# Kernel tuning notes

Hardware: AMD Instinct MI355X
Metric: run time of the kernel (lower is better)

Reference implementation:

```python
import jax, jax.numpy as jnp
import numpy as np

N = 50000   # n_nodes
E = 800000  # n_edges (directed)
D = 64      # feature dim (in = hidden = out = 64 per source)


def setup_inputs() -> dict:
    key = jax.random.key(0)
    ks = jax.random.split(key, 16)
    s = 0.1  # init scale
    inp = {
        "x": jax.random.normal(ks[0], (N, D), jnp.float32),
        "edge_index": jax.random.randint(ks[1], (2, E), 0, N),
        # GCNConv 1
        "W1": jax.random.normal(ks[2], (D, 64), jnp.float32) * s,
        "b1": jnp.zeros((64,), jnp.float32),
        # TransformerConv (heads=1): query/key/value + root (skip) linear
        "Wq": jax.random.normal(ks[3], (64, 64), jnp.float32) * s,
        "bq": jnp.zeros((64,), jnp.float32),
        "Wk": jax.random.normal(ks[4], (64, 64), jnp.float32) * s,
        "bk": jnp.zeros((64,), jnp.float32),
        "Wv": jax.random.normal(ks[5], (64, 64), jnp.float32) * s,
        "bv": jnp.zeros((64,), jnp.float32),
        "Ws": jax.random.normal(ks[6], (64, 64), jnp.float32) * s,
        "bs": jnp.zeros((64,), jnp.float32),
        # GCNConv 2
        "W2": jax.random.normal(ks[7], (64, D), jnp.float32) * s,
        "b2": jnp.zeros((D,), jnp.float32),
    }
    return inp


def gcn_conv(x, W, b, src, dst, n):
    """PyG GCNConv: symmetric normalization with self-loops, then scatter-add."""
    xw = x @ W  # [N, F]
    loop = jnp.arange(n)
    src2 = jnp.concatenate([src, loop])
    dst2 = jnp.concatenate([dst, loop])
    deg = jax.ops.segment_sum(jnp.ones(src2.shape[0], xw.dtype), dst2, num_segments=n)
    dinv = jnp.where(deg > 0, jax.lax.rsqrt(deg), 0.0)
    norm = dinv[src2] * dinv[dst2]  # [E+N]
    out = jax.ops.segment_sum(xw[src2] * norm[:, None], dst2, num_segments=n)
    return out + b


def segment_softmax(logits, seg, n):
    m = jax.ops.segment_max(logits, seg, num_segments=n)
    e = jnp.exp(logits - m[seg])
    z = jax.ops.segment_sum(e, seg, num_segments=n)
    return e / z[seg]


def transformer_conv(x, Wq, bq, Wk, bk, Wv, bv, Ws, bs, src, dst, n):
    """PyG TransformerConv (heads=1, concat=True, root_weight=True)."""
    q = x @ Wq + bq  # [N, 64]
    k = x @ Wk + bk
    v = x @ Wv + bv
    scale = jax.lax.rsqrt(jnp.asarray(q.shape[-1], q.dtype))
    logits = jnp.sum(q[dst] * k[src], axis=-1) * scale  # [E]
    alpha = segment_softmax(logits, dst, n)
    aggr = jax.ops.segment_sum(v[src] * alpha[:, None], dst, num_segments=n)
    return aggr + x @ Ws + bs  # root/skip connection


def reference(x, edge_index, W1, b1, Wq, bq, Wk, bk, Wv, bv, Ws, bs, W2, b2):
    src, dst = edge_index[0], edge_index[1]
    n = x.shape[0]
    x1 = jax.nn.relu(gcn_conv(x, W1, b1, src, dst, n))
    x2 = transformer_conv(x1, Wq, bq, Wk, bk, Wv, bv, Ws, bs, src, dst, n)
    x3 = gcn_conv(x2, W2, b2, src, dst, n)
    return x3
```

## Files before the change

### kernel.cpp

```cpp
#include <hip/hip_runtime.h>
#include <math.h>


#define D 64
#define BKT_SHIFT 9
#define CAP 12288
#define CHUNK 4096

__device__ __forceinline__ unsigned short f2bf(float f) {
    unsigned int u = __float_as_uint(f);
    u += 0x7FFFu + ((u >> 16) & 1u);
    return (unsigned short)(u >> 16);
}
#define BF_LO(u) __uint_as_float((u) << 16)
#define BF_HI(u) __uint_as_float((u) & 0xFFFF0000u)


__global__ void init_gcursor(int* __restrict__ gcursor) {
    if (threadIdx.x < 128) gcursor[threadIdx.x] = 0;
}

__global__ __launch_bounds__(256) void binA_kernel(const int* __restrict__ src,
                                                   const int* __restrict__ dst,
                                                   int* __restrict__ gcursor,
                                                   unsigned int* __restrict__ staging,
                                                   int e, int nbkt) {
    __shared__ int cntB[128];
    __shared__ int offB[128];
    __shared__ int curB[128];
    __shared__ int gbase[128];
    __shared__ unsigned int pairs[CHUNK];
    __shared__ unsigned char bkt[CHUNK];

    int t = threadIdx.x;
    int e0 = blockIdx.x * CHUNK;
    int ecnt = min(CHUNK, e - e0);

    if (t < 128) cntB[t] = 0;
    __syncthreads();

    int myS[CHUNK / 256], myD[CHUNK / 256];
    #pragma unroll
    for (int i = 0; i < CHUNK / 256; ++i) {
        int idx = t + 256 * i;
        if (idx < ecnt) {
            myS[i] = src[e0 + idx];
            myD[i] = dst[e0 + idx];
            atomicAdd(&cntB[myD[i] >> BKT_SHIFT], 1);
        }
    }
    __syncthreads();
    if (t < 128) offB[t] = cntB[t];
    __syncthreads();
    for (int off = 1; off < 128; off <<= 1) {
        int add = (t < 128 && t >= off) ? offB[t - off] : 0;
        __syncthreads();
        if (t < 128) offB[t] += add;
        __syncthreads();
    }
    if (t < 128) {
        int excl = offB[t] - cntB[t];
        offB[t] = excl;
        curB[t] = excl;
        if (t < nbkt && cntB[t] > 0) gbase[t] = atomicAdd(&gcursor[t], cntB[t]);
    }
    __syncthreads();
    #pragma unroll
    for (int i = 0; i < CHUNK / 256; ++i) {
        int idx = t + 256 * i;
        if (idx < ecnt) {
            int b = myD[i] >> BKT_SHIFT;
            int p = atomicAdd(&curB[b], 1);
            pairs[p] = ((unsigned int)myD[i] << 16) | (unsigned int)myS[i];
            bkt[p] = (unsigned char)b;
        }
    }
    __syncthreads();
    for (int p = t; p < ecnt; p += 256) {
        int b = bkt[p];
        staging[(size_t)b * CAP + gbase[b] + (p - offB[b])] = pairs[p];
    }
}

__global__ __launch_bounds__(256) void binB_kernel(const int* __restrict__ gcursor,
                                                   const unsigned int* __restrict__ staging,
                                                   unsigned short* __restrict__ esrc,
                                                   int* __restrict__ cnt,
                                                   int* __restrict__ rowptr,
                                                   float* __restrict__ dinv,
                                                   int n, int nbkt) {
    __shared__ int bpre[128];
    __shared__ int c512[512];
    __shared__ int o512[512];
    int t = threadIdx.x;
    int b = blockIdx.x;

    if (t < 128) bpre[t] = (t < nbkt) ? gcursor[t] : 0;
    __syncthreads();
    for (int off = 1; off < 128; off <<= 1) {
        int add = (t < 128 && t >= off) ? bpre[t - off] : 0;
        __syncthreads();
        if (t < 128) bpre[t] += add;
        __syncthreads();
    }
    int base_b = (b == 0) ? 0 : bpre[b - 1];
    int cnt_b = gcursor[b];
    int lo = b << BKT_SHIFT;

    c512[t] = 0; c512[t + 256] = 0;
    __syncthreads();
    const unsigned int* st = staging + (size_t)b * CAP;
    for (int i = t; i < cnt_b; i += 256)
        atomicAdd(&c512[(int)(st[i] >> 16) - lo], 1);
    __syncthreads();
    o512[t] = c512[t]; o512[t + 256] = c512[t + 256];
    __syncthreads();
    for (int off = 1; off < 512; off <<= 1) {
        int a1 = (t >= off) ? o512[t - off] : 0;
        int a2 = o512[t + 256 - off];
        __syncthreads();
        o512[t] += a1; o512[t + 256] += a2;
        __syncthreads();
    }
    int e1 = o512[t] - c512[t];
    int e2 = o512[t + 256] - c512[t + 256];
    __syncthreads();
    o512[t] = e1; o512[t + 256] = e2;
    __syncthreads();
    for (int i = t; i < 512; i += 256) {
        int g = lo + i;
        if (g < n) {
            int c = c512[i];
            cnt[g] = c;
            rowptr[g] = base_b + o512[i];
            dinv[g] = rsqrtf((float)c + 1.0f);
        }
    }
    __syncthreads();
    for (int i = t; i < cnt_b; i += 256) {
        unsigned int pk = st[i];
        int local = (int)(pk >> 16) - lo;
        int p = atomicAdd(&o512[local], 1);
        esrc[base_b + p] = (unsigned short)(pk & 0xFFFFu);
    }
}

__global__ __launch_bounds__(256) void gemm64_bf16s(const float* __restrict__ X,
                                                    const float* __restrict__ W,
                                                    const float* __restrict__ dinv,
                                                    unsigned short* __restrict__ xs, int n) {
    __shared__ float sX[64][68];
    __shared__ float sW[64 * 64];
    int t = threadIdx.x;
    int base = blockIdx.x * 64;
    #pragma unroll
    for (int i = 0; i < 4; ++i) {
        int f = t * 4 + i * 1024;
        *(float4*)&sW[f] = *(const float4*)&W[f];
        int r = f >> 6, c = f & 63;
        int row = base + r;
        float4 xv = (row < n) ? *(const float4*)&X[(size_t)row * D + c]
                              : make_float4(0.f, 0.f, 0.f, 0.f);
        *(float4*)&sX[r][c] = xv;
    }
    __syncthreads();

    int cg = t & 15, rg = t >> 4;
    int j0 = cg * 4, r0 = rg * 4;
    float acc[4][4];
    #pragma unroll
    for (int a = 0; a < 4; ++a)
        #pragma unroll
        for (int c = 0; c < 4; ++c) acc[a][c] = 0.0f;

    #pragma unroll 4
    for (int kk = 0; kk < 64; kk += 4) {
        float4 w0 = *(const float4*)&sW[(kk + 0) * 64 + j0];
        float4 w1 = *(const float4*)&sW[(kk + 1) * 64 + j0];
        float4 w2 = *(const float4*)&sW[(kk + 2) * 64 + j0];
        float4 w3 = *(const float4*)&sW[(kk + 3) * 64 + j0];
        #pragma unroll
        for (int a = 0; a < 4; ++a) {
            float4 xv = *(const float4*)&sX[r0 + a][kk];
            acc[a][0] = fmaf(xv.x, w0.x, acc[a][0]); acc[a][1] = fmaf(xv.x, w0.y, acc[a][1]);
            acc[a][2] = fmaf(xv.x, w0.z, acc[a][2]); acc[a][3] = fmaf(xv.x, w0.w, acc[a][3]);
            acc[a][0] = fmaf(xv.y, w1.x, acc[a][0]); acc[a][1] = fmaf(xv.y, w1.y, acc[a][1]);
            acc[a][2] = fmaf(xv.y, w1.z, acc[a][2]); acc[a][3] = fmaf(xv.y, w1.w, acc[a][3]);
            acc[a][0] = fmaf(xv.z, w2.x, acc[a][0]); acc[a][1] = fmaf(xv.z, w2.y, acc[a][1]);
            acc[a][2] = fmaf(xv.z, w2.z, acc[a][2]); acc[a][3] = fmaf(xv.z, w2.w, acc[a][3]);
            acc[a][0] = fmaf(xv.w, w3.x, acc[a][0]); acc[a][1] = fmaf(xv.w, w3.y, acc[a][1]);
            acc[a][2] = fmaf(xv.w, w3.z, acc[a][2]); acc[a][3] = fmaf(xv.w, w3.w, acc[a][3]);
        }
    }

    #pragma unroll
    for (int a = 0; a < 4; ++a) {
        int row = base + r0 + a;
        if (row < n) {
            float dv = dinv[row];
            ushort4 h;
            h.x = f2bf(acc[a][0] * dv);
            h.y = f2bf(acc[a][1] * dv);
            h.z = f2bf(acc[a][2] * dv);
            h.w = f2bf(acc[a][3] * dv);
            *(ushort4*)&xs[(size_t)row * D + j0] = h;
        }
    }
}

__global__ __launch_bounds__(256) void fusedA_kernel(const unsigned short* __restrict__ xs,
                                                     const float* __restrict__ dinv,
                                                     const int* __restrict__ rowptr,
                                                     const int* __restrict__ cnt,
                                                     const unsigned short* __restrict__ esrc,
                                                     const float* __restrict__ b1,
                                                     const float* __restrict__ Wq,
                                                     const float* __restrict__ bq,
                                                     const float* __restrict__ Wk,
                                                     const float* __restrict__ bk,
                                                     const float* __restrict__ Wv,
                                                     const float* __restrict__ bv,
                                                     const float* __restrict__ Ws,
                                                     const float* __restrict__ bs,
                                                     float* __restrict__ Yq,
                                                     unsigned short* __restrict__ kv,
                                                     float* __restrict__ Ysk, int n) {
    __shared__ float sX[64][68];
    __shared__ float sW[64 * 64];
    int t = threadIdx.x;
    int base = blockIdx.x * 64;
    int wid = t >> 6, lane = t & 63;
    int grp = lane >> 3, sub = lane & 7;
    int j0 = sub * 8;

    float4 bb0 = *(const float4*)&b1[j0];
    float4 bb1 = *(const float4*)&b1[j0 + 4];

    #pragma unroll
    for (int slot = 0; slot < 2; ++slot) {
        int local = wid * 16 + slot * 8 + grp;
        int node = base + local;
        float a[8] = {0.f, 0.f, 0.f, 0.f, 0.f, 0.f, 0.f, 0.f};
        float4 o0 = make_float4(0.f, 0.f, 0.f, 0.f);
        float4 o1 = make_float4(0.f, 0.f, 0.f, 0.f);
        if (node < n) {
            float dd = dinv[node];
            int start = rowptr[node], deg = cnt[node];
            uint4 sr = *(const uint4*)&xs[(size_t)node * D + j0];
            a[0] += BF_LO(sr.x); a[1] += BF_HI(sr.x);
            a[2] += BF_LO(sr.y); a[3] += BF_HI(sr.y);
            a[4] += BF_LO(sr.z); a[5] += BF_HI(sr.z);
            a[6] += BF_LO(sr.w); a[7] += BF_HI(sr.w);
            int sNext = (deg > 0) ? esrc[start] : 0;
            for (int i = 0; i < deg; ++i) {
                int s = sNext;
                if (i + 1 < deg) sNext = esrc[start + i + 1];
                uint4 r = *(const uint4*)&xs[(size_t)s * D + j0];
                a[0] += BF_LO(r.x); a[1] += BF_HI(r.x);
                a[2] += BF_LO(r.y); a[3] += BF_HI(r.y);
                a[4] += BF_LO(r.z); a[5] += BF_HI(r.z);
                a[6] += BF_LO(r.w); a[7] += BF_HI(r.w);
            }
            o0.x = fmaxf(fmaf(dd, a[0], bb0.x), 0.f);
            o0.y = fmaxf(fmaf(dd, a[1], bb0.y), 0.f);
            o0.z = fmaxf(fmaf(dd, a[2], bb0.z), 0.f);
            o0.w = fmaxf(fmaf(dd, a[3], bb0.w), 0.f);
            o1.x = fmaxf(fmaf(dd, a[4], bb1.x), 0.f);
            o1.y = fmaxf(fmaf(dd, a[5], bb1.y), 0.f);
            o1.z = fmaxf(fmaf(dd, a[6], bb1.z), 0.f);
            o1.w = fmaxf(fmaf(dd, a[7], bb1.w), 0.f);
        }
        *(float4*)&sX[local][j0] = o0;
        *(float4*)&sX[local][j0 + 4] = o1;
    }

    int cg = t & 15, rg = t >> 4;
    int gj0 = cg * 4, r0 = rg * 4;

    #pragma unroll 1
    for (int w4 = 0; w4 < 4; ++w4) {
        const float* W = (w4 == 0) ? Wq : (w4 == 1) ? Wk : (w4 == 2) ? Wv : Ws;
        const float* B = (w4 == 0) ? bq : (w4 == 1) ? bk : (w4 == 2) ? bv : bs;
        __syncthreads();
        #pragma unroll
        for (int i = 0; i < 4; ++i) {
            int f = t * 4 + i * 1024;
            *(float4*)&sW[f] = *(const float4*)&W[f];
        }
        __syncthreads();

        float acc[4][4];
        #pragma unroll
        for (int a = 0; a < 4; ++a)
            #pragma unroll
            for (int c = 0; c < 4; ++c) acc[a][c] = 0.0f;

        #pragma unroll 4
        for (int kk = 0; kk < 64; kk += 4) {
            float4 w0 = *(const float4*)&sW[(kk + 0) * 64 + gj0];
            float4 w1 = *(const float4*)&sW[(kk + 1) * 64 + gj0];
            float4 w2 = *(const float4*)&sW[(kk + 2) * 64 + gj0];
            float4 w3 = *(const float4*)&sW[(kk + 3) * 64 + gj0];
            #pragma unroll
            for (int a = 0; a < 4; ++a) {
                float4 xv = *(const float4*)&sX[r0 + a][kk];
                acc[a][0] = fmaf(xv.x, w0.x, acc[a][0]); acc[a][1] = fmaf(xv.x, w0.y, acc[a][1]);
                acc[a][2] = fmaf(xv.x, w0.z, acc[a][2]); acc[a][3] = fmaf(xv.x, w0.w, acc[a][3]);
                acc[a][0] = fmaf(xv.y, w1.x, acc[a][0]); acc[a][1] = fmaf(xv.y, w1.y, acc[a][1]);
                acc[a][2] = fmaf(xv.y, w1.z, acc[a][2]); acc[a][3] = fmaf(xv.y, w1.w, acc[a][3]);
                acc[a][0] = fmaf(xv.z, w2.x, acc[a][0]); acc[a][1] = fmaf(xv.z, w2.y, acc[a][1]);
                acc[a][2] = fmaf(xv.z, w2.z, acc[a][2]); acc[a][3] = fmaf(xv.z, w2.w, acc[a][3]);
                acc[a][0] = fmaf(xv.w, w3.x, acc[a][0]); acc[a][1] = fmaf(xv.w, w3.y, acc[a][1]);
                acc[a][2] = fmaf(xv.w, w3.z, acc[a][2]); acc[a][3] = fmaf(xv.w, w3.w, acc[a][3]);
            }
        }

        float4 bb = *(const float4*)&B[gj0];
        if (w4 == 0) {
            #pragma unroll
            for (int a = 0; a < 4; ++a) {
                int row = base + r0 + a;
                if (row < n) {
                    float4 o = make_float4((acc[a][0] + bb.x) * 0.125f,
                                           (acc[a][1] + bb.y) * 0.125f,
                                           (acc[a][2] + bb.z) * 0.125f,
                                           (acc[a][3] + bb.w) * 0.125f);
                    *(float4*)&Yq[(size_t)row * D + gj0] = o;
                }
            }
        } else if (w4 == 3) {
            #pragma unroll
            for (int a = 0; a < 4; ++a) {
                int row = base + r0 + a;
                if (row < n) {
                    float4 o = make_float4(acc[a][0] + bb.x, acc[a][1] + bb.y,
                                           acc[a][2] + bb.z, acc[a][3] + bb.w);
                    *(float4*)&Ysk[(size_t)row * D + gj0] = o;
                }
            }
        } else {
            int off = (w4 == 1) ? 0 : 64;
            #pragma unroll
            for (int a = 0; a < 4; ++a) {
                int row = base + r0 + a;
                if (row < n) {
                    ushort4 h;
                    h.x = f2bf(acc[a][0] + bb.x);
                    h.y = f2bf(acc[a][1] + bb.y);
                    h.z = f2bf(acc[a][2] + bb.z);
                    h.w = f2bf(acc[a][3] + bb.w);
                    *(ushort4*)&kv[(size_t)row * 128 + off + gj0] = h;
                }
            }
        }
    }
}

__global__ __launch_bounds__(256) void fusedB_kernel(const float* __restrict__ q,
                                                     const unsigned short* __restrict__ kv,
                                                     const float* __restrict__ skip,
                                                     const float* __restrict__ dinv,
                                                     const int* __restrict__ rowptr,
                                                     const int* __restrict__ cnt,
                                                     const unsigned short* __restrict__ esrc,
                                                     const float* __restrict__ W2,
                                                     unsigned short* __restrict__ xs2, int n) {
    __shared__ float sX[64][68];
    __shared__ float sW[64 * 64];
    int t = threadIdx.x;
    int base = blockIdx.x * 64;
    int wid = t >> 6, lane = t & 63;
    int grp = lane >> 3, sub = lane & 7;
    int j0 = sub * 8;

    #pragma unroll
    for (int i = 0; i < 4; ++i) {
        int f = t * 4 + i * 1024;
        *(float4*)&sW[f] = *(const float4*)&W2[f];
    }

    #pragma unroll
    for (int slot = 0; slot < 2; ++slot) {
        int local = wid * 16 + slot * 8 + grp;
        int node = base + local;
        float4 o0 = make_float4(0.f, 0.f, 0.f, 0.f);
        float4 o1 = make_float4(0.f, 0.f, 0.f, 0.f);
        if (node < n) {
            int start = rowptr[node], deg = cnt[node];
            float4 q0 = *(const float4*)&q[(size_t)node * D + j0];
            float4 q1 = *(const float4*)&q[(size_t)node * D + j0 + 4];
            float4 s0 = *(const float4*)&skip[(size_t)node * D + j0];
            float4 s1 = *(const float4*)&skip[(size_t)node * D + j0 + 4];
            float m = -INFINITY, z = 0.0f;
            float a[8] = {0.f, 0.f, 0.f, 0.f, 0.f, 0.f, 0.f, 0.f};
            int sNext = (deg > 0) ? esrc[start] : 0;
            for (int i = 0; i < deg; ++i) {
                int s = sNext;
                if (i + 1 < deg) sNext = esrc[start + i + 1];
                const unsigned short* row = kv + (size_t)s * 128;
                uint4 kr = *(const uint4*)&row[j0];
                uint4 vr = *(const uint4*)&row[64 + j0];
                float p = q0.x * BF_LO(kr.x) + q0.y * BF_HI(kr.x)
                        + q0.z * BF_LO(kr.y) + q0.w * BF_HI(kr.y)
                        + q1.x * BF_LO(kr.z) + q1.y * BF_HI(kr.z)
                        + q1.z * BF_LO(kr.w) + q1.w * BF_HI(kr.w);
                p += __shfl_xor(p, 1, 64);
                p += __shfl_xor(p, 2, 64);
                p += __shfl_xor(p, 4, 64);
                float mn = fmaxf(m, p);
                float corr = __expf(m - mn);
                float w = __expf(p - mn);
                z = z * corr + w;
                a[0] = fmaf(w, BF_LO(vr.x), a[0] * corr);
                a[1] = fmaf(w, BF_HI(vr.x), a[1] * corr);
                a[2] = fmaf(w, BF_LO(vr.y), a[2] * corr);
                a[3] = fmaf(w, BF_HI(vr.y), a[3] * corr);
                a[4] = fmaf(w, BF_LO(vr.z), a[4] * corr);
                a[5] = fmaf(w, BF_HI(vr.z), a[5] * corr);
                a[6] = fmaf(w, BF_LO(vr.w), a[6] * corr);
                a[7] = fmaf(w, BF_HI(vr.w), a[7] * corr);
                m = mn;
            }
            if (deg > 0) {
                float inv = 1.0f / z;
                o0.x = fmaf(a[0], inv, s0.x); o0.y = fmaf(a[1], inv, s0.y);
                o0.z = fmaf(a[2], inv, s0.z); o0.w = fmaf(a[3], inv, s0.w);
                o1.x = fmaf(a[4], inv, s1.x); o1.y = fmaf(a[5], inv, s1.y);
                o1.z = fmaf(a[6], inv, s1.z); o1.w = fmaf(a[7], inv, s1.w);
            } else {
                o0 = s0; o1 = s1;
            }
        }
        *(float4*)&sX[local][j0] = o0;
        *(float4*)&sX[local][j0 + 4] = o1;
    }
    __syncthreads();

    int cg = t & 15, rg = t >> 4;
    int gj0 = cg * 4, r0 = rg * 4;
    float acc[4][4];
    #pragma unroll
    for (int a = 0; a < 4; ++a)
        #pragma unroll
        for (int c = 0; c < 4; ++c) acc[a][c] = 0.0f;

    #pragma unroll 4
    for (int kk = 0; kk < 64; kk += 4) {
        float4 w0 = *(const float4*)&sW[(kk + 0) * 64 + gj0];
        float4 w1 = *(const float4*)&sW[(kk + 1) * 64 + gj0];
        float4 w2 = *(const float4*)&sW[(kk + 2) * 64 + gj0];
        float4 w3 = *(const float4*)&sW[(kk + 3) * 64 + gj0];
        #pragma unroll
        for (int a = 0; a < 4; ++a) {
            float4 xv = *(const float4*)&sX[r0 + a][kk];
            acc[a][0] = fmaf(xv.x, w0.x, acc[a][0]); acc[a][1] = fmaf(xv.x, w0.y, acc[a][1]);
            acc[a][2] = fmaf(xv.x, w0.z, acc[a][2]); acc[a][3] = fmaf(xv.x, w0.w, acc[a][3]);
            acc[a][0] = fmaf(xv.y, w1.x, acc[a][0]); acc[a][1] = fmaf(xv.y, w1.y, acc[a][1]);
            acc[a][2] = fmaf(xv.y, w1.z, acc[a][2]); acc[a][3] = fmaf(xv.y, w1.w, acc[a][3]);
            acc[a][0] = fmaf(xv.z, w2.x, acc[a][0]); acc[a][1] = fmaf(xv.z, w2.y, acc[a][1]);
            acc[a][2] = fmaf(xv.z, w2.z, acc[a][2]); acc[a][3] = fmaf(xv.z, w2.w, acc[a][3]);
            acc[a][0] = fmaf(xv.w, w3.x, acc[a][0]); acc[a][1] = fmaf(xv.w, w3.y, acc[a][1]);
            acc[a][2] = fmaf(xv.w, w3.z, acc[a][2]); acc[a][3] = fmaf(xv.w, w3.w, acc[a][3]);
        }
    }

    #pragma unroll
    for (int a = 0; a < 4; ++a) {
        int row = base + r0 + a;
        if (row < n) {
            float dv = dinv[row];
            ushort4 h;
            h.x = f2bf(acc[a][0] * dv);
            h.y = f2bf(acc[a][1] * dv);
            h.z = f2bf(acc[a][2] * dv);
            h.w = f2bf(acc[a][3] * dv);
            *(ushort4*)&xs2[(size_t)row * D + gj0] = h;
        }
    }
}

__global__ __launch_bounds__(256) void gcn_gather_kernel(const unsigned short* __restrict__ xs,
                                                         const float* __restrict__ dinv,
                                                         const int* __restrict__ rowptr,
                                                         const int* __restrict__ cnt,
                                                         const unsigned short* __restrict__ esrc,
                                                         const float* __restrict__ bias,
                                                         float* __restrict__ out,
                                                         int n, int relu) {
    int node = (blockIdx.x * blockDim.x + threadIdx.x) >> 6;
    if (node >= n) return;
    int lane = threadIdx.x & 63;
    int grp = lane >> 3;
    int sub = lane & 7;
    int j0 = sub * 8;

    int start = rowptr[node], deg = cnt[node];

    float a[8] = {0.f, 0.f, 0.f, 0.f, 0.f, 0.f, 0.f, 0.f};
    int i = grp;
    int sNext = (i < deg) ? esrc[start + i] : 0;
    for (; i < deg; i += 8) {
        int s = sNext;
        int in = i + 8;
        if (in < deg) sNext = esrc[start + in];
        uint4 r = *(const uint4*)&xs[(size_t)s * D + j0];
        a[0] += BF_LO(r.x); a[1] += BF_HI(r.x);
        a[2] += BF_LO(r.y); a[3] += BF_HI(r.y);
        a[4] += BF_LO(r.z); a[5] += BF_HI(r.z);
        a[6] += BF_LO(r.w); a[7] += BF_HI(r.w);
    }
    #pragma unroll
    for (int off = 8; off < 64; off <<= 1) {
        #pragma unroll
        for (int c = 0; c < 8; ++c) a[c] += __shfl_xor(a[c], off, 64);
    }

    if (grp == 0) {
        float dd = dinv[node];
        uint4 sr = *(const uint4*)&xs[(size_t)node * D + j0];
        a[0] += BF_LO(sr.x); a[1] += BF_HI(sr.x);
        a[2] += BF_LO(sr.y); a[3] += BF_HI(sr.y);
        a[4] += BF_LO(sr.z); a[5] += BF_HI(sr.z);
        a[6] += BF_LO(sr.w); a[7] += BF_HI(sr.w);
        float4 b0 = *(const float4*)&bias[j0];
        float4 b1 = *(const float4*)&bias[j0 + 4];
        float o[8];
        o[0] = fmaf(dd, a[0], b0.x); o[1] = fmaf(dd, a[1], b0.y);
        o[2] = fmaf(dd, a[2], b0.z); o[3] = fmaf(dd, a[3], b0.w);
        o[4] = fmaf(dd, a[4], b1.x); o[5] = fmaf(dd, a[5], b1.y);
        o[6] = fmaf(dd, a[6], b1.z); o[7] = fmaf(dd, a[7], b1.w);
        if (relu) {
            #pragma unroll
            for (int c = 0; c < 8; ++c) o[c] = fmaxf(o[c], 0.f);
        }
        *(float4*)&out[(size_t)node * D + j0] = make_float4(o[0], o[1], o[2], o[3]);
        *(float4*)&out[(size_t)node * D + j0 + 4] = make_float4(o[4], o[5], o[6], o[7]);
    }
}


extern "C" void kernel_launch(void* const* d_in, const int* in_sizes, int n_in,
                              void* d_out, int out_size, void* d_ws, size_t ws_size,
                              hipStream_t stream) {
    const float* x  = (const float*)d_in[0];
    const int*   ei = (const int*)d_in[1];
    const float* W1 = (const float*)d_in[2];
    const float* b1 = (const float*)d_in[3];
    const float* Wq = (const float*)d_in[4];
    const float* bq = (const float*)d_in[5];
    const float* Wk = (const float*)d_in[6];
    const float* bk = (const float*)d_in[7];
    const float* Wv = (const float*)d_in[8];
    const float* bv = (const float*)d_in[9];
    const float* Ws = (const float*)d_in[10];
    const float* bs = (const float*)d_in[11];
    const float* W2 = (const float*)d_in[12];
    const float* b2 = (const float*)d_in[13];
    float* out = (float*)d_out;

    const int n = in_sizes[0] / D;
    const int e = in_sizes[1] / 2;
    const int* src = ei;
    const int* dst = ei + e;
    const int n64 = n * D;
    const int nbkt = (n + (1 << BKT_SHIFT) - 1) >> BKT_SHIFT;

    char* w = (char*)d_ws;
    auto carve = [&](size_t bytes) {
        char* p = w;
        w += (bytes + 255) & ~(size_t)255;
        return p;
    };
    int* gcursor            = (int*)carve(128 * 4);
    unsigned int* staging   = (unsigned int*)carve((size_t)nbkt * CAP * 4);
    unsigned short* esrc    = (unsigned short*)carve((size_t)e * 2);
    int* cnt                = (int*)carve((size_t)n * 4);
    int* rowptr             = (int*)carve((size_t)n * 4);
    float* dinv             = (float*)carve((size_t)n * 4);
    float* bufQ             = (float*)carve((size_t)n64 * 4);
    unsigned short* xs      = (unsigned short*)carve((size_t)n64 * 2);
    unsigned short* kv      = (unsigned short*)carve((size_t)n64 * 4);

    const int nb_binA = (e + CHUNK - 1) / CHUNK;
    const int nb_nw   = (n + 3) / 4;
    const int nb_g    = (n + 63) / 64;

    init_gcursor<<<1, 128, 0, stream>>>(gcursor);
    binA_kernel<<<nb_binA, 256, 0, stream>>>(src, dst, gcursor, staging, e, nbkt);
    binB_kernel<<<nbkt, 256, 0, stream>>>(gcursor, staging, esrc, cnt, rowptr, dinv, n, nbkt);

    gemm64_bf16s<<<nb_g, 256, 0, stream>>>(x, W1, dinv, xs, n);

    fusedA_kernel<<<nb_g, 256, 0, stream>>>(xs, dinv, rowptr, cnt, esrc, b1,
                                            Wq, bq, Wk, bk, Wv, bv, Ws, bs,
                                            bufQ, kv, out, n);

    fusedB_kernel<<<nb_g, 256, 0, stream>>>(bufQ, kv, out, dinv,
                                            rowptr, cnt, esrc, W2, xs, n);

    gcn_gather_kernel<<<nb_nw, 256, 0, stream>>>(xs, dinv, rowptr, cnt, esrc,
                                                 b2, out, n, 0);
}
```

Before: 245.6 us.

## Use 512-thread blocks, unroll neighbor gathers by four, drop online-softmax max tracking

fusedA and fusedB now launch with 512 threads so each 8-lane group handles one node instead of two sequential slots, and the GEMM tiles shrink to 2 rows per thread. Neighbor gathers are unrolled by four so more independent loads are in flight per edge. The attention softmax drops the running maximum and rescaling and accumulates exp(logit) directly. This removes the correction multiplies but risks overflow if logits grow large.

```diff
diff --git a/kernel.cpp b/kernel.cpp
--- a/kernel.cpp
+++ b/kernel.cpp
@@ -208,7 +208,7 @@
     }
 }
 
-__global__ __launch_bounds__(256) void fusedA_kernel(const unsigned short* __restrict__ xs,
+__global__ __launch_bounds__(512) void fusedA_kernel(const unsigned short* __restrict__ xs,
                                                      const float* __restrict__ dinv,
                                                      const int* __restrict__ rowptr,
                                                      const int* __restrict__ cnt,
@@ -229,17 +229,11 @@
     __shared__ float sW[64 * 64];
     int t = threadIdx.x;
     int base = blockIdx.x * 64;
-    int wid = t >> 6, lane = t & 63;
-    int grp = lane >> 3, sub = lane & 7;
+    int local = t >> 3, sub = t & 7;
     int j0 = sub * 8;
-
-    float4 bb0 = *(const float4*)&b1[j0];
-    float4 bb1 = *(const float4*)&b1[j0 + 4];
-
-    #pragma unroll
-    for (int slot = 0; slot < 2; ++slot) {
-        int local = wid * 16 + slot * 8 + grp;
-        int node = base + local;
+    int node = base + local;
+
+    {
         float a[8] = {0.f, 0.f, 0.f, 0.f, 0.f, 0.f, 0.f, 0.f};
         float4 o0 = make_float4(0.f, 0.f, 0.f, 0.f);
         float4 o1 = make_float4(0.f, 0.f, 0.f, 0.f);
@@ -251,16 +245,35 @@
             a[2] += BF_LO(sr.y); a[3] += BF_HI(sr.y);
             a[4] += BF_LO(sr.z); a[5] += BF_HI(sr.z);
             a[6] += BF_LO(sr.w); a[7] += BF_HI(sr.w);
-            int sNext = (deg > 0) ? esrc[start] : 0;
-            for (int i = 0; i < deg; ++i) {
-                int s = sNext;
-                if (i + 1 < deg) sNext = esrc[start + i + 1];
+            int i = 0;
+            for (; i + 4 <= deg; i += 4) {
+                int s0 = esrc[start + i + 0];
+                int s1 = esrc[start + i + 1];
+                int s2 = esrc[start + i + 2];
+                int s3 = esrc[start + i + 3];
+                uint4 r0 = *(const uint4*)&xs[(size_t)s0 * D + j0];
+                uint4 r1 = *(const uint4*)&xs[(size_t)s1 * D + j0];
+                uint4 r2 = *(const uint4*)&xs[(size_t)s2 * D + j0];
+                uint4 r3 = *(const uint4*)&xs[(size_t)s3 * D + j0];
+                a[0] += BF_LO(r0.x) + BF_LO(r1.x) + BF_LO(r2.x) + BF_LO(r3.x);
+                a[1] += BF_HI(r0.x) + BF_HI(r1.x) + BF_HI(r2.x) + BF_HI(r3.x);
+                a[2] += BF_LO(r0.y) + BF_LO(r1.y) + BF_LO(r2.y) + BF_LO(r3.y);
+                a[3] += BF_HI(r0.y) + BF_HI(r1.y) + BF_HI(r2.y) + BF_HI(r3.y);
+                a[4] += BF_LO(r0.z) + BF_LO(r1.z) + BF_LO(r2.z) + BF_LO(r3.z);
+                a[5] += BF_HI(r0.z) + BF_HI(r1.z) + BF_HI(r2.z) + BF_HI(r3.z);
+                a[6] += BF_LO(r0.w) + BF_LO(r1.w) + BF_LO(r2.w) + BF_LO(r3.w);
+                a[7] += BF_HI(r0.w) + BF_HI(r1.w) + BF_HI(r2.w) + BF_HI(r3.w);
+            }
+            for (; i < deg; ++i) {
+                int s = esrc[start + i];
                 uint4 r = *(const uint4*)&xs[(size_t)s * D + j0];
                 a[0] += BF_LO(r.x); a[1] += BF_HI(r.x);
                 a[2] += BF_LO(r.y); a[3] += BF_HI(r.y);
                 a[4] += BF_LO(r.z); a[5] += BF_HI(r.z);
                 a[6] += BF_LO(r.w); a[7] += BF_HI(r.w);
             }
+            float4 bb0 = *(const float4*)&b1[j0];
+            float4 bb1 = *(const float4*)&b1[j0 + 4];
             o0.x = fmaxf(fmaf(dd, a[0], bb0.x), 0.f);
             o0.y = fmaxf(fmaf(dd, a[1], bb0.y), 0.f);
             o0.z = fmaxf(fmaf(dd, a[2], bb0.z), 0.f);
@@ -275,7 +288,7 @@
     }
 
     int cg = t & 15, rg = t >> 4;
-    int gj0 = cg * 4, r0 = rg * 4;
+    int gj0 = cg * 4, r0 = rg * 2;
 
     #pragma unroll 1
     for (int w4 = 0; w4 < 4; ++w4) {
@@ -283,15 +296,15 @@
         const float* B = (w4 == 0) ? bq : (w4 == 1) ? bk : (w4 == 2) ? bv : bs;
         __syncthreads();
         #pragma unroll
-        for (int i = 0; i < 4; ++i) {
-            int f = t * 4 + i * 1024;
+        for (int i = 0; i < 2; ++i) {
+            int f = t * 4 + i * 2048;
             *(float4*)&sW[f] = *(const float4*)&W[f];
         }
         __syncthreads();
 
-        float acc[4][4];
+        float acc[2][4];
         #pragma unroll
-        for (int a = 0; a < 4; ++a)
+        for (int a = 0; a < 2; ++a)
             #pragma unroll
             for (int c = 0; c < 4; ++c) acc[a][c] = 0.0f;
 
@@ -302,7 +315,7 @@
             float4 w2 = *(const float4*)&sW[(kk + 2) * 64 + gj0];
             float4 w3 = *(const float4*)&sW[(kk + 3) * 64 + gj0];
             #pragma unroll
-            for (int a = 0; a < 4; ++a) {
+            for (int a = 0; a < 2; ++a) {
                 float4 xv = *(const float4*)&sX[r0 + a][kk];
                 acc[a][0] = fmaf(xv.x, w0.x, acc[a][0]); acc[a][1] = fmaf(xv.x, w0.y, acc[a][1]);
                 acc[a][2] = fmaf(xv.x, w0.z, acc[a][2]); acc[a][3] = fmaf(xv.x, w0.w, acc[a][3]);
@@ -318,7 +331,7 @@
         float4 bb = *(const float4*)&B[gj0];
         if (w4 == 0) {
             #pragma unroll
-            for (int a = 0; a < 4; ++a) {
+            for (int a = 0; a < 2; ++a) {
                 int row = base + r0 + a;
                 if (row < n) {
                     float4 o = make_float4((acc[a][0] + bb.x) * 0.125f,
@@ -330,7 +343,7 @@
             }
         } else if (w4 == 3) {
             #pragma unroll
-            for (int a = 0; a < 4; ++a) {
+            for (int a = 0; a < 2; ++a) {
                 int row = base + r0 + a;
                 if (row < n) {
                     float4 o = make_float4(acc[a][0] + bb.x, acc[a][1] + bb.y,
@@ -341,7 +354,7 @@
         } else {
             int off = (w4 == 1) ? 0 : 64;
             #pragma unroll
-            for (int a = 0; a < 4; ++a) {
+            for (int a = 0; a < 2; ++a) {
                 int row = base + r0 + a;
                 if (row < n) {
                     ushort4 h;
@@ -356,7 +369,7 @@
     }
 }
 
-__global__ __launch_bounds__(256) void fusedB_kernel(const float* __restrict__ q,
+__global__ __launch_bounds__(512) void fusedB_kernel(const float* __restrict__ q,
                                                      const unsigned short* __restrict__ kv,
                                                      const float* __restrict__ skip,
                                                      const float* __restrict__ dinv,
@@ -369,20 +382,17 @@
     __shared__ float sW[64 * 64];
     int t = threadIdx.x;
     int base = blockIdx.x * 64;
-    int wid = t >> 6, lane = t & 63;
-    int grp = lane >> 3, sub = lane & 7;
+    int local = t >> 3, sub = t & 7;
     int j0 = sub * 8;
-
-    #pragma unroll
-    for (int i = 0; i < 4; ++i) {
-        int f = t * 4 + i * 1024;
+    int node = base + local;
+
+    #pragma unroll
+    for (int i = 0; i < 2; ++i) {
+        int f = t * 4 + i * 2048;
         *(float4*)&sW[f] = *(const float4*)&W2[f];
     }
 
-    #pragma unroll
-    for (int slot = 0; slot < 2; ++slot) {
-        int local = wid * 16 + slot * 8 + grp;
-        int node = base + local;
+    {
         float4 o0 = make_float4(0.f, 0.f, 0.f, 0.f);
         float4 o1 = make_float4(0.f, 0.f, 0.f, 0.f);
         if (node < n) {
@@ -391,12 +401,62 @@
             float4 q1 = *(const float4*)&q[(size_t)node * D + j0 + 4];
             float4 s0 = *(const float4*)&skip[(size_t)node * D + j0];
             float4 s1 = *(const float4*)&skip[(size_t)node * D + j0 + 4];
-            float m = -INFINITY, z = 0.0f;
+            float z = 0.0f;
             float a[8] = {0.f, 0.f, 0.f, 0.f, 0.f, 0.f, 0.f, 0.f};
-            int sNext = (deg > 0) ? esrc[start] : 0;
-            for (int i = 0; i < deg; ++i) {
-                int s = sNext;
-                if (i + 1 < deg) sNext = esrc[start + i + 1];
+            int i = 0;
+            for (; i + 4 <= deg; i += 4) {
+                int e0 = esrc[start + i + 0];
+                int e1 = esrc[start + i + 1];
+                int e2 = esrc[start + i + 2];
+                int e3 = esrc[start + i + 3];
+                const unsigned short* r0p = kv + (size_t)e0 * 128;
+                const unsigned short* r1p = kv + (size_t)e1 * 128;
+                const unsigned short* r2p = kv + (size_t)e2 * 128;
+                const unsigned short* r3p = kv + (size_t)e3 * 128;
+                uint4 k0 = *(const uint4*)&r0p[j0];
+                uint4 k1 = *(const uint4*)&r1p[j0];
+                uint4 k2 = *(const uint4*)&r2p[j0];
+                uint4 k3 = *(const uint4*)&r3p[j0];
+                uint4 v0 = *(const uint4*)&r0p[64 + j0];
+                uint4 v1 = *(const uint4*)&r1p[64 + j0];
+                uint4 v2 = *(const uint4*)&r2p[64 + j0];
+                uint4 v3 = *(const uint4*)&r3p[64 + j0];
+                float p0 = q0.x * BF_LO(k0.x) + q0.y * BF_HI(k0.x)
+                         + q0.z * BF_LO(k0.y) + q0.w * BF_HI(k0.y)
+                         + q1.x * BF_LO(k0.z) + q1.y * BF_HI(k0.z)
+                         + q1.z * BF_LO(k0.w) + q1.w * BF_HI(k0.w);
+                float p1 = q0.x * BF_LO(k1.x) + q0.y * BF_HI(k1.x)
+                         + q0.z * BF_LO(k1.y) + q0.w * BF_HI(k1.y)
+                         + q1.x * BF_LO(k1.z) + q1.y * BF_HI(k1.z)
+                         + q1.z * BF_LO(k1.w) + q1.w * BF_HI(k1.w);
+                float p2 = q0.x * BF_LO(k2.x) + q0.y * BF_HI(k2.x)
+                         + q0.z * BF_LO(k2.y) + q0.w * BF_HI(k2.y)
+                         + q1.x * BF_LO(k2.z) + q1.y * BF_HI(k2.z)
+                         + q1.z * BF_LO(k2.w) + q1.w * BF_HI(k2.w);
+                float p3 = q0.x * BF_LO(k3.x) + q0.y * BF_HI(k3.x)
+                         + q0.z * BF_LO(k3.y) + q0.w * BF_HI(k3.y)
+                         + q1.x * BF_LO(k3.z) + q1.y * BF_HI(k3.z)
+                         + q1.z * BF_LO(k3.w) + q1.w * BF_HI(k3.w);
+                #pragma unroll
+                for (int off = 1; off < 8; off <<= 1) {
+                    p0 += __shfl_xor(p0, off, 64);
+                    p1 += __shfl_xor(p1, off, 64);
+                    p2 += __shfl_xor(p2, off, 64);
+                    p3 += __shfl_xor(p3, off, 64);
+                }
+                float w0 = __expf(p0), w1 = __expf(p1), w2 = __expf(p2), w3 = __expf(p3);
+                z += (w0 + w1) + (w2 + w3);
+                a[0] += w0 * BF_LO(v0.x) + w1 * BF_LO(v1.x) + w2 * BF_LO(v2.x) + w3 * BF_LO(v3.x);
+                a[1] += w0 * BF_HI(v0.x) + w1 * BF_HI(v1.x) + w2 * BF_HI(v2.x) + w3 * BF_HI(v3.x);
+                a[2] += w0 * BF_LO(v0.y) + w1 * BF_LO(v1.y) + w2 * BF_LO(v2.y) + w3 * BF_LO(v3.y);
+                a[3] += w0 * BF_HI(v0.y) + w1 * BF_HI(v1.y) + w2 * BF_HI(v2.y) + w3 * BF_HI(v3.y);
+                a[4] += w0 * BF_LO(v0.z) + w1 * BF_LO(v1.z) + w2 * BF_LO(v2.z) + w3 * BF_LO(v3.z);
+                a[5] += w0 * BF_HI(v0.z) + w1 * BF_HI(v1.z) + w2 * BF_HI(v2.z) + w3 * BF_HI(v3.z);
+                a[6] += w0 * BF_LO(v0.w) + w1 * BF_LO(v1.w) + w2 * BF_LO(v2.w) + w3 * BF_LO(v3.w);
+                a[7] += w0 * BF_HI(v0.w) + w1 * BF_HI(v1.w) + w2 * BF_HI(v2.w) + w3 * BF_HI(v3.w);
+            }
+            for (; i < deg; ++i) {
+                int s = esrc[start + i];
                 const unsigned short* row = kv + (size_t)s * 128;
                 uint4 kr = *(const uint4*)&row[j0];
                 uint4 vr = *(const uint4*)&row[64 + j0];
@@ -404,22 +464,14 @@
                         + q0.z * BF_LO(kr.y) + q0.w * BF_HI(kr.y)
                         + q1.x * BF_LO(kr.z) + q1.y * BF_HI(kr.z)
                         + q1.z * BF_LO(kr.w) + q1.w * BF_HI(kr.w);
-                p += __shfl_xor(p, 1, 64);
-                p += __shfl_xor(p, 2, 64);
-                p += __shfl_xor(p, 4, 64);
-                float mn = fmaxf(m, p);
-                float corr = __expf(m - mn);
-                float w = __expf(p - mn);
-                z = z * corr + w;
-                a[0] = fmaf(w, BF_LO(vr.x), a[0] * corr);
-                a[1] = fmaf(w, BF_HI(vr.x), a[1] * corr);
-                a[2] = fmaf(w, BF_LO(vr.y), a[2] * corr);
-                a[3] = fmaf(w, BF_HI(vr.y), a[3] * corr);
-                a[4] = fmaf(w, BF_LO(vr.z), a[4] * corr);
-                a[5] = fmaf(w, BF_HI(vr.z), a[5] * corr);
-                a[6] = fmaf(w, BF_LO(vr.w), a[6] * corr);
-                a[7] = fmaf(w, BF_HI(vr.w), a[7] * corr);
-                m = mn;
+                #pragma unroll
+                for (int off = 1; off < 8; off <<= 1) p += __shfl_xor(p, off, 64);
+                float w = __expf(p);
+                z += w;
+                a[0] += w * BF_LO(vr.x); a[1] += w * BF_HI(vr.x);
+                a[2] += w * BF_LO(vr.y); a[3] += w * BF_HI(vr.y);
+                a[4] += w * BF_LO(vr.z); a[5] += w * BF_HI(vr.z);
+                a[6] += w * BF_LO(vr.w); a[7] += w * BF_HI(vr.w);
             }
             if (deg > 0) {
                 float inv = 1.0f / z;
@@ -437,10 +489,10 @@
     __syncthreads();
 
     int cg = t & 15, rg = t >> 4;
-    int gj0 = cg * 4, r0 = rg * 4;
-    float acc[4][4];
-    #pragma unroll
-    for (int a = 0; a < 4; ++a)
+    int gj0 = cg * 4, r0 = rg * 2;
+    float acc[2][4];
+    #pragma unroll
+    for (int a = 0; a < 2; ++a)
         #pragma unroll
         for (int c = 0; c < 4; ++c) acc[a][c] = 0.0f;
 
@@ -451,7 +503,7 @@
         float4 w2 = *(const float4*)&sW[(kk + 2) * 64 + gj0];
         float4 w3 = *(const float4*)&sW[(kk + 3) * 64 + gj0];
         #pragma unroll
-        for (int a = 0; a < 4; ++a) {
+        for (int a = 0; a < 2; ++a) {
             float4 xv = *(const float4*)&sX[r0 + a][kk];
             acc[a][0] = fmaf(xv.x, w0.x, acc[a][0]); acc[a][1] = fmaf(xv.x, w0.y, acc[a][1]);
             acc[a][2] = fmaf(xv.x, w0.z, acc[a][2]); acc[a][3] = fmaf(xv.x, w0.w, acc[a][3]);
@@ -465,7 +517,7 @@
     }
 
     #pragma unroll
-    for (int a = 0; a < 4; ++a) {
+    for (int a = 0; a < 2; ++a) {
         int row = base + r0 + a;
         if (row < n) {
             float dv = dinv[row];
@@ -591,11 +643,11 @@
 
     gemm64_bf16s<<<nb_g, 256, 0, stream>>>(x, W1, dinv, xs, n);
 
-    fusedA_kernel<<<nb_g, 256, 0, stream>>>(xs, dinv, rowptr, cnt, esrc, b1,
+    fusedA_kernel<<<nb_g, 512, 0, stream>>>(xs, dinv, rowptr, cnt, esrc, b1,
                                             Wq, bq, Wk, bk, Wv, bv, Ws, bs,
                                             bufQ, kv, out, n);
 
-    fusedB_kernel<<<nb_g, 256, 0, stream>>>(bufQ, kv, out, dinv,
+    fusedB_kernel<<<nb_g, 512, 0, stream>>>(bufQ, kv, out, dinv,
                                             rowptr, cnt, esrc, W2, xs, n);
 
     gcn_gather_kernel<<<nb_nw, 256, 0, stream>>>(xs, dinv, rowptr, cnt, esrc,
```

Result: slower. 252.2 us (+2.7%).
